# Performance work log

Hardware: AMD Instinct MI355X
Metric: run time of the kernel (lower is better)

Reference implementation:

```python
import jax, jax.numpy as jnp
import numpy as np

B, T, C = 2, 2048, 1024
H, DH = 16, 64  # num_heads, dim_head; inner_dim = H*DH = C


def setup_inputs() -> dict:
    key = jax.random.key(0)
    k_x, k_q, k_k, k_v, k_o, k_r = jax.random.split(key, 6)
    scaled = lambda k, shape, fan: (jax.random.normal(k, shape, jnp.float32) / np.sqrt(fan).astype(np.float32))
    x = jax.random.normal(k_x, (B, T, C), jnp.float32)
    Wq = scaled(k_q, (C, H * DH), C)
    Wk = scaled(k_k, (C, H * DH), C)
    Wv = scaled(k_v, (C, H * DH), C)
    Wo = scaled(k_o, (H * DH, C), H * DH)
    bo = jnp.zeros((C,), jnp.float32)
    # learned relative position bias table, indexed by (i - j) in [-(T-1), T-1]
    rel_table = jax.random.normal(k_r, (H, 2 * T - 1), jnp.float32) * 0.02
    # causal mask, broadcast over batch and heads
    mask = jnp.tril(jnp.ones((T, T), bool))[None, None]  # [1,1,T,T]
    return {"x": x, "Wq": Wq, "Wk": Wk, "Wv": Wv, "Wo": Wo, "bo": bo,
            "rel_table": rel_table, "mask": mask}


def reference(x, Wq, Wk, Wv, Wo, bo, rel_table, mask):
    Bx, Tx, Cx = x.shape
    split = lambda t: t.reshape(Bx, Tx, H, DH).transpose(0, 2, 1, 3)  # [B,H,T,DH]
    q = split(x @ Wq) * (DH ** -0.5)
    k = split(x @ Wk)
    v = split(x @ Wv)
    # relative position bias: bias[h,i,j] = rel_table[h, i-j + T-1]
    rel_idx = jnp.arange(Tx)[:, None] - jnp.arange(Tx)[None, :] + (Tx - 1)  # [T,T]
    bias = rel_table[:, rel_idx]  # [H,T,T]
    score = jnp.einsum('bhid,bhjd->bhij', q, k) + bias[None]
    mask_value = -jnp.finfo(score.dtype).max
    score = jnp.where(mask, score, mask_value)
    attn = jax.nn.softmax(score, axis=-1)
    y = jnp.einsum('bhij,bhjd->bhid', attn, v)
    y = y.transpose(0, 2, 1, 3).reshape(Bx, Tx, H * DH)
    return y @ Wo + bo
```

## Files before the change

kernel.cpp:

```cpp
#include <hip/hip_runtime.h>
#include <hip/hip_bf16.h>
#include <stdint.h>


#define T_SEQ 2048
#define NH    16
#define DHD   64
#define CDIM  1024

typedef unsigned short u16;
typedef unsigned int   u32;
typedef __attribute__((ext_vector_type(8))) __bf16 bf16x8;
typedef __attribute__((ext_vector_type(4))) float f32x4;

#define WAITL0   asm volatile("s_waitcnt lgkmcnt(0)" ::: "memory")

__device__ __forceinline__ float bf2f(u16 b){
  union { u32 u; float f; } v; v.u = ((u32)b) << 16; return v.f;
}
__device__ __forceinline__ u16 f2bf(float f){
  union { __bf16 h; u16 u; } v; v.h = (__bf16)f;
  return v.u;
}

__device__ __forceinline__ uint4 load8(const void* p, long elem, int isbf){
  if (isbf) return *(const uint4*)((const u16*)p + elem);
  const float* fp = (const float*)p + elem;
  float4 a = *(const float4*)fp, b = *(const float4*)(fp + 4);
  uint4 r;
  r.x = (u32)f2bf(a.x) | ((u32)f2bf(a.y) << 16);
  r.y = (u32)f2bf(a.z) | ((u32)f2bf(a.w) << 16);
  r.z = (u32)f2bf(b.x) | ((u32)f2bf(b.y) << 16);
  r.w = (u32)f2bf(b.z) | ((u32)f2bf(b.w) << 16);
  return r;
}
__device__ __forceinline__ float loadf(const void* p, long idx, int isbf){
  return isbf ? bf2f(((const u16*)p)[idx]) : ((const float*)p)[idx];
}

__global__ __launch_bounds__(256) void classify(const u32* __restrict__ x,
                                                int* __restrict__ flag){
  __shared__ int cnt[256];
  int c = 0;
#pragma unroll
  for (int i = 0; i < 16; i++){
    u32 w = x[threadIdx.x * 16 + i];
    int e = (w >> 7) & 0xFF;
    c += (e >= 110 && e <= 140);
  }
  cnt[threadIdx.x] = c;
  __syncthreads();
  for (int s = 128; s > 0; s >>= 1){
    if ((int)threadIdx.x < s) cnt[threadIdx.x] += cnt[threadIdx.x + s];
    __syncthreads();
  }
  if (threadIdx.x == 0) *flag = (cnt[0] > 2048) ? 1 : 0;
}

__global__ __launch_bounds__(256) void transposeW(
    const void* __restrict__ w0, const void* __restrict__ w1,
    const void* __restrict__ w2,
    u16* __restrict__ o0, u16* __restrict__ o1, u16* __restrict__ o2,
    const int* __restrict__ flag)
{
  __shared__ u16 tile[64][72];
  const int isbf = *flag;
  const int z = blockIdx.z;
  const void* in = z==0 ? w0 : z==1 ? w1 : w2;
  u16*      out  = z==0 ? o0 : z==1 ? o1 : o2;
  const int tid = threadIdx.x;
  const int r0 = blockIdx.y * 64, c0 = blockIdx.x * 64;
  const int rr = tid >> 3;
  const int cc = (tid & 7) * 8;
#pragma unroll
  for (int rd = 0; rd < 2; rd++){
    int r = rd*32 + rr;
    *(uint4*)&tile[r][cc] = load8(in, (long)(r0 + r)*CDIM + c0 + cc, isbf);
  }
  __syncthreads();
#pragma unroll
  for (int rd = 0; rd < 2; rd++){
    int oc = rd*32 + rr;
    uint4 wv; u32* wp = (u32*)&wv;
#pragma unroll
    for (int t = 0; t < 4; t++){
      u32 lo = tile[cc + 2*t][oc];
      u32 hi = tile[cc + 2*t + 1][oc];
      wp[t] = lo | (hi << 16);
    }
    *(uint4*)(out + (long)(c0 + oc)*CDIM + r0 + cc) = wv;
  }
}

__device__ __forceinline__ void gemm_body(
    const void* __restrict__ A, const u16* __restrict__ BT,
    const void* __restrict__ bias, void* __restrict__ out,
    float scale, int mode, int m0, int n0, int a_isbf, int io_isbf)
{
  __shared__ u16 ldsA[128*32];
  __shared__ u16 ldsB[128*32];
  const int tid = threadIdx.x;
  const int wid = tid >> 6, lane = tid & 63;
  const int col = lane & 15, quad = lane >> 4;
  const int wm = (wid >> 1) * 64, wn = (wid & 1) * 64;

  const int r0s = tid >> 2, g0 = tid & 3;
  const int r1s = r0s + 64;
  const int sl0 = (g0 ^ (r0s & 3)) * 8;
  const int sl1 = (g0 ^ (r1s & 3)) * 8;

  uint4 rA0, rA1, rB0, rB1;
  auto loadAB = [&](int k0){
    rA0 = load8(A, (long)(m0 + r0s)*CDIM + k0 + g0*8, a_isbf);
    rA1 = load8(A, (long)(m0 + r1s)*CDIM + k0 + g0*8, a_isbf);
    rB0 = *(const uint4*)(BT + (long)(n0 + r0s)*CDIM + k0 + g0*8);
    rB1 = *(const uint4*)(BT + (long)(n0 + r1s)*CDIM + k0 + g0*8);
  };
  auto storeAB = [&](){
    *(uint4*)&ldsA[r0s*32 + sl0] = rA0;
    *(uint4*)&ldsA[r1s*32 + sl1] = rA1;
    *(uint4*)&ldsB[r0s*32 + sl0] = rB0;
    *(uint4*)&ldsB[r1s*32 + sl1] = rB1;
  };

  f32x4 acc[4][4] = {};
  const int NK = CDIM / 32;

  loadAB(0);
  storeAB();
  __syncthreads();

  for (int k = 0; k < NK; k++){
    if (k + 1 < NK) loadAB((k + 1) * 32);

    bf16x8 af[4], bfr[4];
#pragma unroll
    for (int mi = 0; mi < 4; mi++){
      const int r = wm + mi*16 + col;
      af[mi] = *(const bf16x8*)&ldsA[r*32 + ((quad ^ (r & 3)) * 8)];
    }
#pragma unroll
    for (int ni = 0; ni < 4; ni++){
      const int r = wn + ni*16 + col;
      bfr[ni] = *(const bf16x8*)&ldsB[r*32 + ((quad ^ (r & 3)) * 8)];
    }
#pragma unroll
    for (int mi = 0; mi < 4; mi++)
#pragma unroll
      for (int ni = 0; ni < 4; ni++)
        acc[mi][ni] = __builtin_amdgcn_mfma_f32_16x16x32_bf16(af[mi], bfr[ni], acc[mi][ni], 0, 0, 0);

    __syncthreads();
    if (k + 1 < NK){
      storeAB();
      __syncthreads();
    }
  }

  if (mode == 2){
#pragma unroll
    for (int ni = 0; ni < 4; ni++){
      const int n = n0 + wn + ni*16 + col;
      const int h = n >> 6, d = n & 63;
#pragma unroll
      for (int mi = 0; mi < 4; mi++){
        const int m = m0 + wm + mi*16 + quad*4;
        const int b = m >> 11, t = m & (T_SEQ-1);
        uint2 pk;
        pk.x = (u32)f2bf(acc[mi][ni][0]) | ((u32)f2bf(acc[mi][ni][1]) << 16);
        pk.y = (u32)f2bf(acc[mi][ni][2]) | ((u32)f2bf(acc[mi][ni][3]) << 16);
        *(uint2*)((u16*)out + ((long)(b*NH + h)*DHD + d)*T_SEQ + t) = pk;
      }
    }
  } else {
#pragma unroll
    for (int ni = 0; ni < 4; ni++){
      const int n = n0 + wn + ni*16 + col;
      const float bv = bias ? loadf(bias, n, io_isbf) : 0.f;
#pragma unroll
      for (int mi = 0; mi < 4; mi++){
#pragma unroll
        for (int r = 0; r < 4; r++){
          const int m = m0 + wm + mi*16 + quad*4 + r;
          const float v = acc[mi][ni][r] * scale + bv;
          if (mode == 0){
            const long idx = (long)m*CDIM + n;
            if (io_isbf) ((u16*)out)[idx] = f2bf(v);
            else         ((float*)out)[idx] = v;
          } else {
            const int b = m >> 11, t = m & (T_SEQ-1), h = n >> 6, d = n & 63;
            ((u16*)out)[((long)(b*NH + h)*T_SEQ + t)*DHD + d] = f2bf(v);
          }
        }
      }
    }
  }
}

__global__ __launch_bounds__(256) void gemm_qkv(
    const void* __restrict__ x,
    const u16* __restrict__ WqT, const u16* __restrict__ WkT, const u16* __restrict__ WvT,
    u16* __restrict__ Qb, u16* __restrict__ Kb, u16* __restrict__ VTb,
    const int* __restrict__ flag)
{
  const int z = blockIdx.z;
  const u16* BT = z==0 ? WqT : z==1 ? WkT : WvT;
  u16*      dst = z==0 ? Qb  : z==1 ? Kb  : VTb;
  const float scale = (z==0) ? 0.125f * 1.44269504f : 1.0f;
  const int mode = (z==2) ? 2 : 1;
  gemm_body(x, BT, nullptr, dst, scale, mode, blockIdx.x*128, blockIdx.y*128, *flag, 1);
}

__global__ __launch_bounds__(256) void gemm_out(
    const u16* __restrict__ Y, const u16* __restrict__ WoT,
    const void* __restrict__ bo, void* __restrict__ out,
    const int* __restrict__ flag)
{
  gemm_body(Y, WoT, bo, out, 1.0f, 0, blockIdx.x*128, blockIdx.y*128, 1, *flag);
}

__global__ __launch_bounds__(256) void attn64(
    const u16* __restrict__ Q, const u16* __restrict__ K, const u16* __restrict__ VT,
    const void* __restrict__ rel, u16* __restrict__ Y,
    const int* __restrict__ flag)
{
  __shared__ u16 ldsK[64*64];
  __shared__ u16 ldsV[64*64];
  __shared__ u16 ldsP[4][16*88];
  __shared__ float ldsBias[2112];

  const int isbf = *flag;
  const int tid = threadIdx.x, wid = tid >> 6, lane = tid & 63;
  const int col = lane & 15, quad = lane >> 4;

  const int l = (int)blockIdx.x + 16 * (int)blockIdx.y;
  const int xcd = l & 7, s = l >> 3;
  const int bh = xcd * 4 + (s & 3);
  const int bx = s >> 2;

  const int h = bh & (NH - 1);
  const int b = bh >> 4;

  const u16* Qh = Q  + (long)bh * T_SEQ * DHD;
  const u16* Kh = K  + (long)bh * T_SEQ * DHD;
  const u16* Vh = VT + (long)bh * DHD * T_SEQ;
  const long relbase = (long)h * (2*T_SEQ - 1) + (T_SEQ - 1);
  const float MLOG = 16.0f * 1.44269504f;

  const int kr0 = tid >> 3, ks = tid & 7;
  const int kr1 = kr0 + 32;
  const int kd0 = (ks ^ (kr0 & 7)) * 8;
  const int kd1 = (ks ^ (kr1 & 7)) * 8;

  uint4 rk0, rk1, rv0, rv1;
  auto loadKV = [&](int j0){
    rk0 = *(const uint4*)(Kh + (long)(j0 + kr0)*DHD + ks*8);
    rk1 = *(const uint4*)(Kh + (long)(j0 + kr1)*DHD + ks*8);
    rv0 = *(const uint4*)(Vh + (long)kr0*T_SEQ + j0 + ks*8);
    rv1 = *(const uint4*)(Vh + (long)kr1*T_SEQ + j0 + ks*8);
  };
  auto storeKV = [&](){
    *(uint4*)&ldsK[kr0*64 + kd0] = rk0;
    *(uint4*)&ldsK[kr1*64 + kd1] = rk1;
    *(uint4*)&ldsV[kr0*64 + kd0] = rv0;
    *(uint4*)&ldsV[kr1*64 + kd1] = rv1;
  };

  for (int ph = 0; ph < 2; ph++){
    const int ti = ph ? (31 - bx) : bx;
    const int i0 = ti * 64;
    if (ph) __syncthreads();

    const int nbias = i0 + 127;
    for (int t = tid; t < nbias; t += 256)
      ldsBias[t] = loadf(rel, relbase + t - 63, isbf) * 1.44269504f - MLOG;

    bf16x8 qf0, qf1;
    {
      const u16* qp = Qh + (long)(i0 + wid*16 + col)*DHD + quad*8;
      qf0 = *(const bf16x8*)qp;
      qf1 = *(const bf16x8*)(qp + 32);
    }

    f32x4 O[4] = {};
    float lsum[4] = {0.f, 0.f, 0.f, 0.f};
    const int irow = i0 + wid*16 + quad*4;

    loadKV(0);
    storeKV();
    __syncthreads();

    for (int j0 = 0; j0 <= i0; j0 += 64){
      const bool have_next = (j0 + 64 <= i0);
      if (have_next) loadKV(j0 + 64);

      f32x4 s[4] = {};
#pragma unroll
      for (int kb = 0; kb < 2; kb++){
#pragma unroll
        for (int nb = 0; nb < 4; nb++){
          const int row = nb*16 + col;
          const int sl = ((kb*4 + quad) ^ (row & 7)) * 8;
          bf16x8 kf = *(const bf16x8*)&ldsK[row*64 + sl];
          s[nb] = __builtin_amdgcn_mfma_f32_16x16x32_bf16(kb ? qf1 : qf0, kf, s[nb], 0, 0, 0);
        }
      }

      const bool diag = (j0 == i0);
#pragma unroll
      for (int nb = 0; nb < 4; nb++){
        const int j = j0 + nb*16 + col;
        const float* bp = &ldsBias[irow - j + 63];
#pragma unroll
        for (int r = 0; r < 4; r++){
          float arg = s[nb][r] + bp[r];
          if (diag && (j > irow + r)) arg = -1e9f;
          float p;
          asm volatile("v_exp_f32 %0, %1" : "=v"(p) : "v"(arg));
          s[nb][r] = p;
          lsum[r] += p;
        }
      }

      u16* Pw = ldsP[wid];
#pragma unroll
      for (int nb = 0; nb < 4; nb++)
#pragma unroll
        for (int r = 0; r < 4; r++)
          Pw[(quad*4 + r)*88 + nb*16 + col] = f2bf(s[nb][r]);
      WAITL0;

#pragma unroll
      for (int kb = 0; kb < 2; kb++){
        bf16x8 pf = *(const bf16x8*)&Pw[col*88 + kb*32 + quad*8];
#pragma unroll
        for (int nb = 0; nb < 4; nb++){
          const int row = nb*16 + col;
          const int sl = ((kb*4 + quad) ^ (row & 7)) * 8;
          bf16x8 vf = *(const bf16x8*)&ldsV[row*64 + sl];
          O[nb] = __builtin_amdgcn_mfma_f32_16x16x32_bf16(pf, vf, O[nb], 0, 0, 0);
        }
      }

      __syncthreads();
      if (have_next){
        storeKV();
        __syncthreads();
      }
    }

#pragma unroll
    for (int r = 0; r < 4; r++){
      float v = lsum[r];
      v += __shfl_xor(v, 1, 64);
      v += __shfl_xor(v, 2, 64);
      v += __shfl_xor(v, 4, 64);
      v += __shfl_xor(v, 8, 64);
      lsum[r] = v;
    }

#pragma unroll
    for (int nb = 0; nb < 4; nb++){
#pragma unroll
      for (int r = 0; r < 4; r++){
        const int i = irow + r;
        const int d = nb*16 + col;
        Y[((long)(b*T_SEQ + i))*CDIM + h*DHD + d] = f2bf(O[nb][r] / lsum[r]);
      }
    }
  }
}

extern "C" void kernel_launch(void* const* d_in, const int* in_sizes, int n_in,
                              void* d_out, int out_size, void* d_ws, size_t ws_size,
                              hipStream_t stream)
{
  (void)in_sizes; (void)n_in; (void)out_size; (void)ws_size;
  const void* x   = d_in[0];
  const void* Wq  = d_in[1];
  const void* Wk  = d_in[2];
  const void* Wv  = d_in[3];
  const void* Wo  = d_in[4];
  const void* bo  = d_in[5];
  const void* rel = d_in[6];

  char* ws = (char*)d_ws;
  const size_t MB = 1024*1024;
  int* flag = (int*)ws;
  char* base = ws + 256;
  u16* WqT = (u16*)(base + 0*MB);
  u16* WkT = (u16*)(base + 2*MB);
  u16* WvT = (u16*)(base + 4*MB);
  u16* Kb  = (u16*)(base + 6*MB);
  u16* VTb = (u16*)(base + 14*MB);
  u16* Yb  = (u16*)(base + 0*MB);
  u16* WoT = (u16*)(base + 8*MB);
  u16* Qb  = (u16*)d_out;

  dim3 blk(256);
  classify  <<<1, blk, 0, stream>>>((const u32*)x, flag);
  transposeW<<<dim3(16,16,3), blk, 0, stream>>>(Wq, Wk, Wv, WqT, WkT, WvT, flag);
  gemm_qkv  <<<dim3(32,8,3),  blk, 0, stream>>>(x, WqT, WkT, WvT, Qb, Kb, VTb, flag);
  attn64    <<<dim3(16,32),   blk, 0, stream>>>(Qb, Kb, VTb, rel, Yb, flag);
  transposeW<<<dim3(16,16,1), blk, 0, stream>>>(Wo, Wo, Wo, WoT, WoT, WoT, flag);
  gemm_out  <<<dim3(32,8),    blk, 0, stream>>>(Yb, WoT, bo, d_out, flag);
}
```

Before: 245.4 us.

## Split attention into 1024 two-wave blocks and inline dtype classification

Drops the separate classify kernel: each kernel now detects the input dtype itself with a wave ballot over 64 words of x. The attention kernel becomes one 64-row query tile per 128-thread block, with each wave handling 32 rows (two 16-row MFMA tiles) so each K/V fragment read from LDS is reused twice. The grid grows to 1024 blocks with an XCD-aware mapping that pairs causal tiles for load balance, replacing the two-phase loop inside each block. Risks are higher register pressure, fewer waves to hide latency, and a dtype check that samples far fewer words than before.

```diff
diff --git a/kernel.cpp b/kernel.cpp
--- a/kernel.cpp
+++ b/kernel.cpp
@@ -21,6 +21,13 @@
 __device__ __forceinline__ u16 f2bf(float f){
   union { __bf16 h; u16 u; } v; v.h = (__bf16)f;
   return v.u;
+}
+
+__device__ __forceinline__ int classify_x(const u32* xw){
+  u32 w = xw[threadIdx.x & 63];
+  int e = (w >> 7) & 0xFF;
+  unsigned long long m = __ballot(e >= 110 && e <= 140);
+  return __popcll(m) > 32;
 }
 
 __device__ __forceinline__ uint4 load8(const void* p, long elem, int isbf){
@@ -38,33 +45,14 @@
   return isbf ? bf2f(((const u16*)p)[idx]) : ((const float*)p)[idx];
 }
 
-__global__ __launch_bounds__(256) void classify(const u32* __restrict__ x,
-                                                int* __restrict__ flag){
-  __shared__ int cnt[256];
-  int c = 0;
-#pragma unroll
-  for (int i = 0; i < 16; i++){
-    u32 w = x[threadIdx.x * 16 + i];
-    int e = (w >> 7) & 0xFF;
-    c += (e >= 110 && e <= 140);
-  }
-  cnt[threadIdx.x] = c;
-  __syncthreads();
-  for (int s = 128; s > 0; s >>= 1){
-    if ((int)threadIdx.x < s) cnt[threadIdx.x] += cnt[threadIdx.x + s];
-    __syncthreads();
-  }
-  if (threadIdx.x == 0) *flag = (cnt[0] > 2048) ? 1 : 0;
-}
-
 __global__ __launch_bounds__(256) void transposeW(
     const void* __restrict__ w0, const void* __restrict__ w1,
     const void* __restrict__ w2,
     u16* __restrict__ o0, u16* __restrict__ o1, u16* __restrict__ o2,
-    const int* __restrict__ flag)
+    const u32* __restrict__ xw)
 {
   __shared__ u16 tile[64][72];
-  const int isbf = *flag;
+  const int isbf = classify_x(xw);
   const int z = blockIdx.z;
   const void* in = z==0 ? w0 : z==1 ? w1 : w2;
   u16*      out  = z==0 ? o0 : z==1 ? o1 : o2;
@@ -200,46 +188,49 @@
 __global__ __launch_bounds__(256) void gemm_qkv(
     const void* __restrict__ x,
     const u16* __restrict__ WqT, const u16* __restrict__ WkT, const u16* __restrict__ WvT,
-    u16* __restrict__ Qb, u16* __restrict__ Kb, u16* __restrict__ VTb,
-    const int* __restrict__ flag)
-{
+    u16* __restrict__ Qb, u16* __restrict__ Kb, u16* __restrict__ VTb)
+{
+  const int isbf = classify_x((const u32*)x);
   const int z = blockIdx.z;
   const u16* BT = z==0 ? WqT : z==1 ? WkT : WvT;
   u16*      dst = z==0 ? Qb  : z==1 ? Kb  : VTb;
   const float scale = (z==0) ? 0.125f * 1.44269504f : 1.0f;
   const int mode = (z==2) ? 2 : 1;
-  gemm_body(x, BT, nullptr, dst, scale, mode, blockIdx.x*128, blockIdx.y*128, *flag, 1);
+  gemm_body(x, BT, nullptr, dst, scale, mode, blockIdx.x*128, blockIdx.y*128, isbf, 1);
 }
 
 __global__ __launch_bounds__(256) void gemm_out(
     const u16* __restrict__ Y, const u16* __restrict__ WoT,
     const void* __restrict__ bo, void* __restrict__ out,
-    const int* __restrict__ flag)
-{
-  gemm_body(Y, WoT, bo, out, 1.0f, 0, blockIdx.x*128, blockIdx.y*128, 1, *flag);
-}
-
-__global__ __launch_bounds__(256) void attn64(
+    const u32* __restrict__ xw)
+{
+  const int isbf = classify_x(xw);
+  gemm_body(Y, WoT, bo, out, 1.0f, 0, blockIdx.x*128, blockIdx.y*128, 1, isbf);
+}
+
+__global__ __launch_bounds__(128) void attn64(
     const u16* __restrict__ Q, const u16* __restrict__ K, const u16* __restrict__ VT,
     const void* __restrict__ rel, u16* __restrict__ Y,
-    const int* __restrict__ flag)
+    const u32* __restrict__ xw)
 {
   __shared__ u16 ldsK[64*64];
   __shared__ u16 ldsV[64*64];
-  __shared__ u16 ldsP[4][16*88];
+  __shared__ u16 ldsP[2][32*88];
   __shared__ float ldsBias[2112];
 
-  const int isbf = *flag;
+  const int isbf = classify_x(xw);
   const int tid = threadIdx.x, wid = tid >> 6, lane = tid & 63;
   const int col = lane & 15, quad = lane >> 4;
 
-  const int l = (int)blockIdx.x + 16 * (int)blockIdx.y;
-  const int xcd = l & 7, s = l >> 3;
-  const int bh = xcd * 4 + (s & 3);
-  const int bx = s >> 2;
-
+  const int l = (int)blockIdx.x;
+  const int xcd = l & 7, v = l >> 3;
+  const int u = v & 31, hl = v >> 5;
+  const int base = (u + ((hl >> 1) << 4)) & 31;
+  const int bx = (hl & 1) ? (31 - base) : base;
+  const int bh = xcd * 4 + hl;
   const int h = bh & (NH - 1);
   const int b = bh >> 4;
+  const int i0 = bx * 64;
 
   const u16* Qh = Q  + (long)bh * T_SEQ * DHD;
   const u16* Kh = K  + (long)bh * T_SEQ * DHD;
@@ -247,125 +238,136 @@
   const long relbase = (long)h * (2*T_SEQ - 1) + (T_SEQ - 1);
   const float MLOG = 16.0f * 1.44269504f;
 
-  const int kr0 = tid >> 3, ks = tid & 7;
-  const int kr1 = kr0 + 32;
-  const int kd0 = (ks ^ (kr0 & 7)) * 8;
-  const int kd1 = (ks ^ (kr1 & 7)) * 8;
-
-  uint4 rk0, rk1, rv0, rv1;
+  const int nbias = i0 + 127;
+  for (int t = tid; t < nbias; t += 128)
+    ldsBias[t] = loadf(rel, relbase + t - 63, isbf) * 1.44269504f - MLOG;
+
+  bf16x8 qf[2][2];
+#pragma unroll
+  for (int rb = 0; rb < 2; rb++){
+    const u16* qp = Qh + (long)(i0 + wid*32 + rb*16 + col)*DHD + quad*8;
+    qf[rb][0] = *(const bf16x8*)qp;
+    qf[rb][1] = *(const bf16x8*)(qp + 32);
+  }
+
+  const int kr = tid >> 3, ks = tid & 7;
+  const int kd = (ks ^ (kr & 7)) * 8;
+  uint4 rk[4], rv[4];
   auto loadKV = [&](int j0){
-    rk0 = *(const uint4*)(Kh + (long)(j0 + kr0)*DHD + ks*8);
-    rk1 = *(const uint4*)(Kh + (long)(j0 + kr1)*DHD + ks*8);
-    rv0 = *(const uint4*)(Vh + (long)kr0*T_SEQ + j0 + ks*8);
-    rv1 = *(const uint4*)(Vh + (long)kr1*T_SEQ + j0 + ks*8);
+#pragma unroll
+    for (int c = 0; c < 4; c++){
+      rk[c] = *(const uint4*)(Kh + (long)(j0 + kr + 16*c)*DHD + ks*8);
+      rv[c] = *(const uint4*)(Vh + (long)(kr + 16*c)*T_SEQ + j0 + ks*8);
+    }
   };
   auto storeKV = [&](){
-    *(uint4*)&ldsK[kr0*64 + kd0] = rk0;
-    *(uint4*)&ldsK[kr1*64 + kd1] = rk1;
-    *(uint4*)&ldsV[kr0*64 + kd0] = rv0;
-    *(uint4*)&ldsV[kr1*64 + kd1] = rv1;
+#pragma unroll
+    for (int c = 0; c < 4; c++){
+      *(uint4*)&ldsK[(kr + 16*c)*64 + kd] = rk[c];
+      *(uint4*)&ldsV[(kr + 16*c)*64 + kd] = rv[c];
+    }
   };
 
-  for (int ph = 0; ph < 2; ph++){
-    const int ti = ph ? (31 - bx) : bx;
-    const int i0 = ti * 64;
-    if (ph) __syncthreads();
-
-    const int nbias = i0 + 127;
-    for (int t = tid; t < nbias; t += 256)
-      ldsBias[t] = loadf(rel, relbase + t - 63, isbf) * 1.44269504f - MLOG;
-
-    bf16x8 qf0, qf1;
-    {
-      const u16* qp = Qh + (long)(i0 + wid*16 + col)*DHD + quad*8;
-      qf0 = *(const bf16x8*)qp;
-      qf1 = *(const bf16x8*)(qp + 32);
-    }
-
-    f32x4 O[4] = {};
-    float lsum[4] = {0.f, 0.f, 0.f, 0.f};
-    const int irow = i0 + wid*16 + quad*4;
-
-    loadKV(0);
-    storeKV();
-    __syncthreads();
-
-    for (int j0 = 0; j0 <= i0; j0 += 64){
-      const bool have_next = (j0 + 64 <= i0);
-      if (have_next) loadKV(j0 + 64);
-
-      f32x4 s[4] = {};
-#pragma unroll
-      for (int kb = 0; kb < 2; kb++){
-#pragma unroll
-        for (int nb = 0; nb < 4; nb++){
-          const int row = nb*16 + col;
-          const int sl = ((kb*4 + quad) ^ (row & 7)) * 8;
-          bf16x8 kf = *(const bf16x8*)&ldsK[row*64 + sl];
-          s[nb] = __builtin_amdgcn_mfma_f32_16x16x32_bf16(kb ? qf1 : qf0, kf, s[nb], 0, 0, 0);
-        }
-      }
-
-      const bool diag = (j0 == i0);
+  f32x4 O[2][4] = {};
+  float lsum[2][4] = {};
+  const int irow0 = i0 + wid*32 + quad*4;
+
+  loadKV(0);
+  storeKV();
+  __syncthreads();
+
+  for (int j0 = 0; j0 <= i0; j0 += 64){
+    const bool have_next = (j0 + 64 <= i0);
+    if (have_next) loadKV(j0 + 64);
+
+    f32x4 s[2][4] = {};
+#pragma unroll
+    for (int kb = 0; kb < 2; kb++){
+#pragma unroll
+      for (int nb = 0; nb < 4; nb++){
+        const int row = nb*16 + col;
+        const int sl = ((kb*4 + quad) ^ (row & 7)) * 8;
+        bf16x8 kf = *(const bf16x8*)&ldsK[row*64 + sl];
+#pragma unroll
+        for (int rb = 0; rb < 2; rb++)
+          s[rb][nb] = __builtin_amdgcn_mfma_f32_16x16x32_bf16(qf[rb][kb], kf, s[rb][nb], 0, 0, 0);
+      }
+    }
+
+    const bool diag = (j0 == i0);
+#pragma unroll
+    for (int rb = 0; rb < 2; rb++){
+      const int ir = irow0 + rb*16;
 #pragma unroll
       for (int nb = 0; nb < 4; nb++){
         const int j = j0 + nb*16 + col;
-        const float* bp = &ldsBias[irow - j + 63];
+        const float* bp = &ldsBias[ir - j + 63];
 #pragma unroll
         for (int r = 0; r < 4; r++){
-          float arg = s[nb][r] + bp[r];
-          if (diag && (j > irow + r)) arg = -1e9f;
-          float p;
-          asm volatile("v_exp_f32 %0, %1" : "=v"(p) : "v"(arg));
-          s[nb][r] = p;
-          lsum[r] += p;
+          float arg = s[rb][nb][r] + bp[r];
+          if (diag && (j > ir + r)) arg = -1e9f;
+          float p = exp2f(arg);
+          s[rb][nb][r] = p;
+          lsum[rb][r] += p;
         }
       }
-
-      u16* Pw = ldsP[wid];
+    }
+
+    u16* Pw = ldsP[wid];
+#pragma unroll
+    for (int rb = 0; rb < 2; rb++)
 #pragma unroll
       for (int nb = 0; nb < 4; nb++)
 #pragma unroll
         for (int r = 0; r < 4; r++)
-          Pw[(quad*4 + r)*88 + nb*16 + col] = f2bf(s[nb][r]);
-      WAITL0;
-
-#pragma unroll
-      for (int kb = 0; kb < 2; kb++){
-        bf16x8 pf = *(const bf16x8*)&Pw[col*88 + kb*32 + quad*8];
-#pragma unroll
-        for (int nb = 0; nb < 4; nb++){
-          const int row = nb*16 + col;
-          const int sl = ((kb*4 + quad) ^ (row & 7)) * 8;
-          bf16x8 vf = *(const bf16x8*)&ldsV[row*64 + sl];
-          O[nb] = __builtin_amdgcn_mfma_f32_16x16x32_bf16(pf, vf, O[nb], 0, 0, 0);
-        }
-      }
-
+          Pw[(rb*16 + quad*4 + r)*88 + nb*16 + col] = f2bf(s[rb][nb][r]);
+    WAITL0;
+
+#pragma unroll
+    for (int kb = 0; kb < 2; kb++){
+      bf16x8 pf[2];
+#pragma unroll
+      for (int rb = 0; rb < 2; rb++)
+        pf[rb] = *(const bf16x8*)&Pw[(rb*16 + col)*88 + kb*32 + quad*8];
+#pragma unroll
+      for (int nb = 0; nb < 4; nb++){
+        const int row = nb*16 + col;
+        const int sl = ((kb*4 + quad) ^ (row & 7)) * 8;
+        bf16x8 vf = *(const bf16x8*)&ldsV[row*64 + sl];
+#pragma unroll
+        for (int rb = 0; rb < 2; rb++)
+          O[rb][nb] = __builtin_amdgcn_mfma_f32_16x16x32_bf16(pf[rb], vf, O[rb][nb], 0, 0, 0);
+      }
+    }
+
+    __syncthreads();
+    if (have_next){
+      storeKV();
       __syncthreads();
-      if (have_next){
-        storeKV();
-        __syncthreads();
-      }
-    }
-
+    }
+  }
+
+#pragma unroll
+  for (int rb = 0; rb < 2; rb++)
 #pragma unroll
     for (int r = 0; r < 4; r++){
-      float v = lsum[r];
-      v += __shfl_xor(v, 1, 64);
-      v += __shfl_xor(v, 2, 64);
-      v += __shfl_xor(v, 4, 64);
-      v += __shfl_xor(v, 8, 64);
-      lsum[r] = v;
-    }
-
+      float vv = lsum[rb][r];
+      vv += __shfl_xor(vv, 1, 64);
+      vv += __shfl_xor(vv, 2, 64);
+      vv += __shfl_xor(vv, 4, 64);
+      vv += __shfl_xor(vv, 8, 64);
+      lsum[rb][r] = vv;
+    }
+
+#pragma unroll
+  for (int rb = 0; rb < 2; rb++){
 #pragma unroll
     for (int nb = 0; nb < 4; nb++){
 #pragma unroll
       for (int r = 0; r < 4; r++){
-        const int i = irow + r;
+        const int i = irow0 + rb*16 + r;
         const int d = nb*16 + col;
-        Y[((long)(b*T_SEQ + i))*CDIM + h*DHD + d] = f2bf(O[nb][r] / lsum[r]);
+        Y[((long)(b*T_SEQ + i))*CDIM + h*DHD + d] = f2bf(O[rb][nb][r] / lsum[rb][r]);
       }
     }
   }
@@ -386,7 +388,6 @@
 
   char* ws = (char*)d_ws;
   const size_t MB = 1024*1024;
-  int* flag = (int*)ws;
   char* base = ws + 256;
   u16* WqT = (u16*)(base + 0*MB);
   u16* WkT = (u16*)(base + 2*MB);
@@ -396,12 +397,11 @@
   u16* Yb  = (u16*)(base + 0*MB);
   u16* WoT = (u16*)(base + 8*MB);
   u16* Qb  = (u16*)d_out;
-
-  dim3 blk(256);
-  classify  <<<1, blk, 0, stream>>>((const u32*)x, flag);
-  transposeW<<<dim3(16,16,3), blk, 0, stream>>>(Wq, Wk, Wv, WqT, WkT, WvT, flag);
-  gemm_qkv  <<<dim3(32,8,3),  blk, 0, stream>>>(x, WqT, WkT, WvT, Qb, Kb, VTb, flag);
-  attn64    <<<dim3(16,32),   blk, 0, stream>>>(Qb, Kb, VTb, rel, Yb, flag);
-  transposeW<<<dim3(16,16,1), blk, 0, stream>>>(Wo, Wo, Wo, WoT, WoT, WoT, flag);
-  gemm_out  <<<dim3(32,8),    blk, 0, stream>>>(Yb, WoT, bo, d_out, flag);
-}
+  const u32* xw = (const u32*)x;
+
+  transposeW<<<dim3(16,16,3), dim3(256), 0, stream>>>(Wq, Wk, Wv, WqT, WkT, WvT, xw);
+  gemm_qkv  <<<dim3(32,8,3),  dim3(256), 0, stream>>>(x, WqT, WkT, WvT, Qb, Kb, VTb);
+  attn64    <<<dim3(1024),    dim3(128), 0, stream>>>(Qb, Kb, VTb, rel, Yb, xw);
+  transposeW<<<dim3(16,16,1), dim3(256), 0, stream>>>(Wo, Wo, Wo, WoT, WoT, WoT, xw);
+  gemm_out  <<<dim3(32,8),    dim3(256), 0, stream>>>(Yb, WoT, bo, d_out, xw);
+}
```

New measurement: 298.4 us. 21.6% more time.
